# Optimization experiments

Measured on AMD Instinct MI355X. Metric: run time of the kernel, lower is better.

Reference implementation:

```python
import jax, jax.numpy as jnp
import numpy as np

L, B, D, N = 2048, 8, 1024, 64

def setup_inputs() -> dict:
    key = jax.random.key(0)
    ks = jax.random.split(key, 6)
    return {
        "x": jax.random.normal(ks[0], (L, B, D), dtype=jnp.float32),
        "damping_factor": jax.random.normal(ks[1], (D, N, 1), dtype=jnp.float32),
        "decay_factor": jax.random.normal(ks[2], (D, N, 1), dtype=jnp.float32),
        "ema_expansion_matrix": jax.random.normal(ks[3], (D, N, 1), dtype=jnp.float32),
        "kernel_projection_matrix": jax.random.normal(ks[4], (D, N), dtype=jnp.float32),
        "residual_weight": jax.random.normal(ks[5], (D,), dtype=jnp.float32),
    }

def reference(x, damping_factor, decay_factor, ema_expansion_matrix,
              kernel_projection_matrix, residual_weight):
    seq_len, bsz, dim = x.shape
    ndim = damping_factor.shape[1]
    # --- kernel synthesis (training path, unidirectional) ---
    damping = jax.nn.sigmoid(damping_factor)           # (D, N, 1)
    decay = jax.nn.sigmoid(decay_factor)               # (D, N, 1)
    prev_w = 1.0 - damping * decay                     # (D, N, 1), in (0,1)
    t = jnp.arange(seq_len, dtype=jnp.float32)[None, None, :]  # (1,1,L)
    vander = t * jnp.log(prev_w)                       # (D, N, L)
    kernel_vals = damping * ema_expansion_matrix * jnp.exp(vander)  # (D,N,L)
    kernel = jnp.einsum('dnl,dn->dl', kernel_vals, kernel_projection_matrix)
    kernel = kernel * np.float32(1.0 / np.sqrt(ndim))  # (D, L)
    # --- residual + FFT long convolution ---
    residual = x * residual_weight                     # (L, B, D)
    x_conv = jnp.transpose(x, (1, 2, 0))               # (B, D, L)
    n_fft = 2 * seq_len
    x_fft = jnp.fft.rfft(x_conv, n=n_fft)              # (B, D, n/2+1)
    k_fft = jnp.fft.rfft(kernel, n=n_fft)              # (D, n/2+1)
    conv = jnp.fft.irfft(x_fft * k_fft, n=n_fft)[..., :seq_len]  # (B, D, L)
    ema_out = jnp.transpose(conv, (2, 0, 1))           # (L, B, D)
    return jax.nn.silu(ema_out + residual)
```

## Files before the change

kernel.cpp:

```cpp
#include <hip/hip_runtime.h>
#include <hip/hip_bf16.h>


#define BSZ 8
#define DIM 1024
#define ND 64
#define BD 8192
#define SEGS 4
#define SEGLEN 512
#define CH1 64
#define CPS1 8
#define TD 16
#define XP1 68
#define NCH2 16
#define YP2 17

typedef short bf16x8 __attribute__((ext_vector_type(8)));
typedef float f32x4 __attribute__((ext_vector_type(4)));
union BF8 { uint32_t u[4]; bf16x8 v; };
#define MFMA __builtin_amdgcn_mfma_f32_16x16x32_bf16

__device__ __forceinline__ uint32_t pk_bf16(float a, float b) {
    __hip_bfloat162 h2 = __float22bfloat162_rn(make_float2(a, b));
    uint32_t u; __builtin_memcpy(&u, &h2, 4);
    return u;
}

__device__ __forceinline__ void block_sync_lds() {
    asm volatile("s_waitcnt lgkmcnt(0)" ::: "memory");
    __builtin_amdgcn_s_barrier();
    asm volatile("" ::: "memory");
}

__global__ __launch_bounds__(128, 8) void mega_pass1(
    const float* __restrict__ x,
    const float* __restrict__ dfp,
    const float* __restrict__ cfp,
    ushort* __restrict__ S)
{
    __shared__ float xb[2][TD * XP1];

    const int tid = threadIdx.x;
    const int lane = tid & 63;
    const int wv = tid >> 6;
    const int q   = (lane & 3) | (((lane >> 3) & 1) << 2);
    const int col = wv * 8 + ((lane >> 2) & 1) + ((lane >> 4) & 3) * 2;
    const int blk = blockIdx.x;
    const int dt  = blk & 63;
    const int b   = (blk >> 6) & 7;
    const int seg = blk >> 9;
    const int d   = dt * TD + col;

    float w[8];
    {
        const int pb = d * ND + q * 8;
        const float4 df0 = *(const float4*)(dfp + pb);
        const float4 df1 = *(const float4*)(dfp + pb + 4);
        const float4 cf0 = *(const float4*)(cfp + pb);
        const float4 cf1 = *(const float4*)(cfp + pb + 4);
        const float dfv[8] = {df0.x, df0.y, df0.z, df0.w, df1.x, df1.y, df1.z, df1.w};
        const float cfv[8] = {cf0.x, cf0.y, cf0.z, cf0.w, cf1.x, cf1.y, cf1.z, cf1.w};
        #pragma unroll
        for (int i = 0; i < 8; ++i) {
            const float sd = 1.0f / (1.0f + __expf(-dfv[i]));
            const float sc = 1.0f / (1.0f + __expf(-cfv[i]));
            w[i] = 1.0f - sd * sc;
        }
    }

    const int r0 = tid >> 2;
    const int c4 = (tid & 3) * 4;
    const float* xg = x + (size_t)(seg * SEGLEN) * BD + b * DIM + dt * TD;

    float4 nx0 = *(const float4*)(xg + (size_t)r0 * BD + c4);
    float4 nx1 = *(const float4*)(xg + (size_t)(r0 + 32) * BD + c4);

    float h[8];
    #pragma unroll
    for (int i = 0; i < 8; ++i) h[i] = 0.0f;

    for (int g = 0; g < CPS1; ++g) {
        float* xbuf = xb[g & 1];
        const float nv0[4] = {nx0.x, nx0.y, nx0.z, nx0.w};
        const float nv1[4] = {nx1.x, nx1.y, nx1.z, nx1.w};
        #pragma unroll
        for (int e = 0; e < 4; ++e) {
            xbuf[(c4 + e) * XP1 + r0]      = nv0[e];
            xbuf[(c4 + e) * XP1 + r0 + 32] = nv1[e];
        }
        if (g + 1 < CPS1) {
            nx0 = *(const float4*)(xg + (size_t)((g + 1) * CH1 + r0) * BD + c4);
            nx1 = *(const float4*)(xg + (size_t)((g + 1) * CH1 + r0 + 32) * BD + c4);
        }
        block_sync_lds();

        const float* xcol = xbuf + col * XP1;
        #pragma unroll 2
        for (int t8 = 0; t8 < 8; ++t8) {
            const float4 tva = *(const float4*)(xcol + t8 * 8);
            const float4 tvb = *(const float4*)(xcol + t8 * 8 + 4);
            const float tvs[8] = {tva.x, tva.y, tva.z, tva.w,
                                  tvb.x, tvb.y, tvb.z, tvb.w};
            #pragma unroll
            for (int k = 0; k < 8; ++k) {
                const float xv = tvs[k];
                #pragma unroll
                for (int i = 0; i < 8; ++i) h[i] = fmaf(w[i], h[i], xv);
            }
        }
    }

    const size_t sb = ((size_t)(seg * BSZ + b) * 64 + dt) * 1024 + col * 64 + q * 8;
    uint32_t pk[4] = {pk_bf16(h[0], h[1]), pk_bf16(h[2], h[3]),
                      pk_bf16(h[4], h[5]), pk_bf16(h[6], h[7])};
    *(uint4*)(S + sb) = make_uint4(pk[0], pk[1], pk[2], pk[3]);
}

__global__ __launch_bounds__(1024, 4) void mega_pass2(
    const float* __restrict__ x,
    const float* __restrict__ dfp,
    const float* __restrict__ cfp,
    const float* __restrict__ emp,
    const float* __restrict__ pjp,
    const float* __restrict__ rwp,
    const ushort* __restrict__ S,
    float* __restrict__ out)
{
    __shared__ __align__(16) ushort   xbh[2][TD * 8 * 32];
    __shared__ __align__(16) float    yt[2][256 * YP2];
    __shared__ __align__(16) uint32_t hbq[16 * 256];
    __shared__ __align__(8)  float2   pclw[16 * 64];
    __shared__ float kap[16 * 32];

    const int tid = threadIdx.x;
    const int tl  = tid & 63;
    const int wv  = tid >> 6;
    const int c   = tl & 15;
    const int g   = tl >> 4;
    const int cq  = c & 7;
    const int hf  = c >> 3;
    const int blk = blockIdx.x;
    const int seg = blk >> 6;
    const int dt  = blk & 63;
    const int d0  = dt * TD;
    const int d   = d0 + wv;

    {
        const int pidx = d * ND + tl;
        const float sd = 1.0f / (1.0f + __expf(-dfp[pidx]));
        const float sc = 1.0f / (1.0f + __expf(-cfp[pidx]));
        const float wn = 1.0f - sd * sc;
        const float cn = sd * emp[pidx] * pjp[pidx] * 0.125f;
        pclw[wv * 64 + tl] = make_float2(cn, log2f(wn));
    }
    const float rwd = rwp[d];

    const int drow = tid & 15;
    const int bq   = ((tid >> 4) & 1) | (((tid >> 6) & 1) << 1) | (((tid >> 8) & 1) << 2);
    const int l4g  = ((tid >> 5) & 1) | (((tid >> 7) & 1) << 1) | (((tid >> 9) & 1) << 2);
    const int Gst  = l4g >> 1;
    const int Hst  = l4g & 1;
    const int Kst  = ((bq >> 1) & 3) ^ (drow & 3);
    const int xwoff = (drow * 8 + bq) * 32 + ((Gst ^ Kst) << 3) + Hst * 4;
    const float* xgs = x + (size_t)(seg * SEGLEN + 4 * l4g) * BD + bq * DIM + d0 + drow;
    float nx0 = xgs[0];
    float nx1 = xgs[(size_t)BD];
    float nx2 = xgs[(size_t)2 * BD];
    float nx3 = xgs[(size_t)3 * BD];

    const int dq  = tid & 3;
    const int b_s = (tid >> 2) & 7;
    const int u_s = (tid >> 5) & 7;
    const int r_s = tid >> 8;
    const int yrow = b_s + 8 * u_s + 64 * r_s;
    const int lam  = 4 * u_s + r_s;

    float lw16[16];
    #pragma unroll
    for (int T = 0; T < 4; ++T)
        #pragma unroll
        for (int r = 0; r < 4; ++r)
            lw16[T * 4 + r] = pclw[wv * 64 + 16 * T + 4 * g + r].y;

    float h[16];
    #pragma unroll
    for (int i = 0; i < 16; ++i) h[i] = 0.0f;
    if (seg > 0) {
        float w512[16];
        #pragma unroll
        for (int i = 0; i < 16; ++i) w512[i] = exp2f(512.0f * lw16[i]);
        for (int sp = 0; sp < seg; ++sp) {
            const size_t sbase = ((size_t)(sp * BSZ + cq) * 64 + dt) * 1024 + wv * 64;
            #pragma unroll
            for (int T = 0; T < 4; ++T) {
                const uint2 u = *(const uint2*)(S + sbase + 16 * T + 4 * g);
                const float s0 = __uint_as_float(u.x << 16);
                const float s1 = __uint_as_float(u.x & 0xFFFF0000u);
                const float s2 = __uint_as_float(u.y << 16);
                const float s3 = __uint_as_float(u.y & 0xFFFF0000u);
                h[T*4+0] = fmaf(w512[T*4+0], h[T*4+0], s0);
                h[T*4+1] = fmaf(w512[T*4+1], h[T*4+1], s1);
                h[T*4+2] = fmaf(w512[T*4+2], h[T*4+2], s2);
                h[T*4+3] = fmaf(w512[T*4+3], h[T*4+3], s3);
            }
        }
    }
    float w32[16];
    #pragma unroll
    for (int i = 0; i < 16; ++i) w32[i] = exp2f(32.0f * lw16[i]);

    BF8 Vf[4], T2f[2][2], Kf[2];
    #pragma unroll
    for (int T = 0; T < 4; ++T) {
        const float2 pcl = pclw[wv * 64 + 16 * T + c];
        const float winv = exp2f(-pcl.y);
        float ve = exp2f((float)(31 - 8 * g) * pcl.y);
        float vv[8];
        #pragma unroll
        for (int e = 0; e < 8; ++e) { vv[e] = ve; ve *= winv; }
        #pragma unroll
        for (int j = 0; j < 4; ++j) Vf[T].u[j] = pk_bf16(vv[2*j], vv[2*j+1]);
    }
    #pragma unroll
    for (int Tk = 0; Tk < 2; ++Tk) {
        float2 m8[8];
        #pragma unroll
        for (int e = 0; e < 8; ++e) m8[e] = pclw[wv * 64 + 32 * Tk + 8 * g + e];
        #pragma unroll
        for (int Tj = 0; Tj < 2; ++Tj) {
            const float jf = (float)(16 * Tj + c + 1);
            float tv[8];
            #pragma unroll
            for (int e = 0; e < 8; ++e) tv[e] = m8[e].x * exp2f(jf * m8[e].y);
            #pragma unroll
            for (int j = 0; j < 4; ++j) T2f[Tj][Tk].u[j] = pk_bf16(tv[2*j], tv[2*j+1]);
        }
    }
    {
        const int p = tl >> 1, half = tl & 1;
        float acc = 0.0f;
        for (int i = 0; i < 32; ++i) {
            const float2 pc = pclw[wv * 64 + half * 32 + i];
            acc = fmaf(pc.x, exp2f((float)p * pc.y), acc);
        }
        const int prt = __builtin_amdgcn_update_dpp(0, __float_as_int(acc), 0xB1, 0xF, 0xF, true);
        acc += __int_as_float(prt);
        if (!half) kap[wv * 32 + p] = acc;
    }
    #pragma unroll
    for (int Tj = 0; Tj < 2; ++Tj) {
        float kv[8];
        #pragma unroll
        for (int e = 0; e < 8; ++e) {
            const int pp = 16 * Tj + c - 8 * g - e;
            float kv_;
            if (pp > 0)       kv_ = kap[wv * 32 + pp];
            else if (pp == 0) kv_ = kap[wv * 32] + rwd;
            else              kv_ = 0.0f;
            kv[e] = kv_;
        }
        #pragma unroll
        for (int j = 0; j < 4; ++j) Kf[Tj].u[j] = pk_bf16(kv[2*j], kv[2*j+1]);
    }

    const int Krd   = ((cq >> 1) & 3) ^ (wv & 3);
    const int xroff = (wv * 8 + cq) * 32 + ((g ^ Krd) << 3);
    const int swzc = ((c & 3) << 3) | (((c >> 2) & 1) << 2);
    uint32_t* hbw = hbq + wv * 256 + cq * 32;
    float* ogbase = out + (size_t)(seg * SEGLEN) * BD + d0;
    const f32x4 zf = {0.0f, 0.0f, 0.0f, 0.0f};

    if (hf == 0) {
        #pragma unroll
        for (int T = 0; T < 4; ++T) {
            const int p0 = 8 * T + 2 * g;
            *(uint2*)(&hbw[p0 ^ swzc]) =
                make_uint2(pk_bf16(h[4*T+0], h[4*T+1]), pk_bf16(h[4*T+2], h[4*T+3]));
        }
    }
    BF8 hB0, hB1;
    {
        const uint4 a  = *(const uint4*)(&hbw[(4 * g) ^ swzc]);
        const uint4 b2 = *(const uint4*)(&hbw[(16 + 4 * g) ^ swzc]);
        hB0.u[0]=a.x;  hB0.u[1]=a.y;  hB0.u[2]=a.z;  hB0.u[3]=a.w;
        hB1.u[0]=b2.x; hB1.u[1]=b2.y; hB1.u[2]=b2.z; hB1.u[3]=b2.w;
    }
    {
        *(uint2*)(&xbh[0][xwoff]) = make_uint2(pk_bf16(nx0, nx1), pk_bf16(nx2, nx3));
        const float* xp = xgs + (size_t)32 * BD;
        nx0 = xp[0]; nx1 = xp[(size_t)BD]; nx2 = xp[(size_t)2*BD]; nx3 = xp[(size_t)3*BD];
    }
    block_sync_lds();

    for (int ch = 0; ch < NCH2; ++ch) {
        BF8 xB;
        xB.v = *(const bf16x8*)(&xbh[ch & 1][xroff]);

        if (ch + 1 < NCH2) {
            *(uint2*)(&xbh[(ch + 1) & 1][xwoff]) =
                make_uint2(pk_bf16(nx0, nx1), pk_bf16(nx2, nx3));
            if (ch + 2 < NCH2) {
                const float* xp = xgs + (size_t)(ch + 2) * 32 * BD;
                nx0 = xp[0]; nx1 = xp[(size_t)BD]; nx2 = xp[(size_t)2*BD]; nx3 = xp[(size_t)3*BD];
            }
        }
        if (ch > 0) {
            const float* yprev = yt[(ch - 1) & 1];
            float ov[4];
            #pragma unroll
            for (int e = 0; e < 4; ++e) ov[e] = yprev[yrow * YP2 + 4 * dq + e];
            *(float4*)(ogbase + (size_t)((ch - 1) * 32 + lam) * BD + b_s * DIM + 4 * dq) =
                make_float4(ov[0], ov[1], ov[2], ov[3]);
        }

        f32x4 y0 = MFMA(Kf[0].v, xB.v, zf, 0, 0, 0);
        f32x4 y1 = MFMA(Kf[1].v, xB.v, zf, 0, 0, 0);
        y0 = MFMA(T2f[0][0].v, hB0.v, y0, 0, 0, 0);
        y1 = MFMA(T2f[1][0].v, hB0.v, y1, 0, 0, 0);
        y0 = MFMA(T2f[0][1].v, hB1.v, y0, 0, 0, 0);
        y1 = MFMA(T2f[1][1].v, hB1.v, y1, 0, 0, 0);
        #pragma unroll
        for (int T = 0; T < 4; ++T) {
            const f32x4 U = MFMA(Vf[T].v, xB.v, zf, 0, 0, 0);
            h[4*T+0] = fmaf(w32[4*T+0], h[4*T+0], U[0]);
            h[4*T+1] = fmaf(w32[4*T+1], h[4*T+1], U[1]);
            h[4*T+2] = fmaf(w32[4*T+2], h[4*T+2], U[2]);
            h[4*T+3] = fmaf(w32[4*T+3], h[4*T+3], U[3]);
        }
        if (hf == 0) {
            #pragma unroll
            for (int T = 0; T < 4; ++T) {
                const int p0 = 8 * T + 2 * g;
                *(uint2*)(&hbw[p0 ^ swzc]) =
                    make_uint2(pk_bf16(h[4*T+0], h[4*T+1]), pk_bf16(h[4*T+2], h[4*T+3]));
            }
        }
        {
            const uint4 a  = *(const uint4*)(&hbw[(4 * g) ^ swzc]);
            const uint4 b2 = *(const uint4*)(&hbw[(16 + 4 * g) ^ swzc]);
            hB0.u[0]=a.x;  hB0.u[1]=a.y;  hB0.u[2]=a.z;  hB0.u[3]=a.w;
            hB1.u[0]=b2.x; hB1.u[1]=b2.y; hB1.u[2]=b2.z; hB1.u[3]=b2.w;
        }

        {
            float* ycur = yt[ch & 1];
            const f32x4 yy = hf ? y1 : y0;
            #pragma unroll
            for (int r = 0; r < 4; ++r) {
                const float v = yy[r];
                const float sv = v / (1.0f + __expf(-v));
                ycur[(cq + 8 * g + 32 * hf + 64 * r) * YP2 + wv] = sv;
            }
        }
        block_sync_lds();
    }

    {
        const float* yprev = yt[(NCH2 - 1) & 1];
        float ov[4];
        #pragma unroll
        for (int e = 0; e < 4; ++e) ov[e] = yprev[yrow * YP2 + 4 * dq + e];
        *(float4*)(ogbase + (size_t)((NCH2 - 1) * 32 + lam) * BD + b_s * DIM + 4 * dq) =
            make_float4(ov[0], ov[1], ov[2], ov[3]);
    }
}

extern "C" void kernel_launch(void* const* d_in, const int* in_sizes, int n_in,
                              void* d_out, int out_size, void* d_ws, size_t ws_size,
                              hipStream_t stream) {
    const float* x  = (const float*)d_in[0];
    const float* df = (const float*)d_in[1];
    const float* cf = (const float*)d_in[2];
    const float* em = (const float*)d_in[3];
    const float* pj = (const float*)d_in[4];
    const float* rw = (const float*)d_in[5];
    float* out = (float*)d_out;
    ushort* S  = (ushort*)d_ws;

    mega_pass1<<<dim3((SEGS - 1) * BSZ * 64), dim3(128), 0, stream>>>(x, df, cf, S);
    mega_pass2<<<dim3(SEGS * 64), dim3(1024), 0, stream>>>(x, df, cf, em, pj, rw, S, out);
}
```

Measured before the change: 75.99 us.

## Preload whole x segment into LDS and store outputs directly without barriers

Stages all 16 chunks of the x segment into LDS as bf16 in one upfront loop, replacing the double-buffered register prefetch. The staging tile for the output transpose is removed: each lane writes its SiLU results straight to global memory. This takes out the per-chunk block barriers and LDS round-trips. In exchange, LDS use grows to roughly 150KB per block. Global stores become 4-byte scattered writes with a DIM stride instead of coalesced float4 stores, and x loads no longer overlap with the MFMA loop.

```diff
diff --git a/kernel.cpp b/kernel.cpp
--- a/kernel.cpp
+++ b/kernel.cpp
@@ -13,7 +13,6 @@
 #define TD 16
 #define XP1 68
 #define NCH2 16
-#define YP2 17
 
 typedef short bf16x8 __attribute__((ext_vector_type(8)));
 typedef float f32x4 __attribute__((ext_vector_type(4)));
@@ -126,8 +125,7 @@
     const ushort* __restrict__ S,
     float* __restrict__ out)
 {
-    __shared__ __align__(16) ushort   xbh[2][TD * 8 * 32];
-    __shared__ __align__(16) float    yt[2][256 * YP2];
+    __shared__ __align__(16) ushort   xbh[NCH2 * TD * 8 * 32];
     __shared__ __align__(16) uint32_t hbq[16 * 256];
     __shared__ __align__(8)  float2   pclw[16 * 64];
     __shared__ float kap[16 * 32];
@@ -163,17 +161,16 @@
     const int Kst  = ((bq >> 1) & 3) ^ (drow & 3);
     const int xwoff = (drow * 8 + bq) * 32 + ((Gst ^ Kst) << 3) + Hst * 4;
     const float* xgs = x + (size_t)(seg * SEGLEN + 4 * l4g) * BD + bq * DIM + d0 + drow;
-    float nx0 = xgs[0];
-    float nx1 = xgs[(size_t)BD];
-    float nx2 = xgs[(size_t)2 * BD];
-    float nx3 = xgs[(size_t)3 * BD];
-
-    const int dq  = tid & 3;
-    const int b_s = (tid >> 2) & 7;
-    const int u_s = (tid >> 5) & 7;
-    const int r_s = tid >> 8;
-    const int yrow = b_s + 8 * u_s + 64 * r_s;
-    const int lam  = 4 * u_s + r_s;
+
+    #pragma unroll 4
+    for (int ch = 0; ch < NCH2; ++ch) {
+        const float* xp = xgs + (size_t)ch * 32 * BD;
+        const float a0 = xp[0];
+        const float a1 = xp[(size_t)BD];
+        const float a2 = xp[(size_t)2 * BD];
+        const float a3 = xp[(size_t)3 * BD];
+        *(uint2*)(&xbh[ch * 4096 + xwoff]) = make_uint2(pk_bf16(a0, a1), pk_bf16(a2, a3));
+    }
 
     float lw16[16];
     #pragma unroll
@@ -263,13 +260,9 @@
         for (int j = 0; j < 4; ++j) Kf[Tj].u[j] = pk_bf16(kv[2*j], kv[2*j+1]);
     }
 
-    const int Krd   = ((cq >> 1) & 3) ^ (wv & 3);
-    const int xroff = (wv * 8 + cq) * 32 + ((g ^ Krd) << 3);
     const int swzc = ((c & 3) << 3) | (((c >> 2) & 1) << 2);
     uint32_t* hbw = hbq + wv * 256 + cq * 32;
-    float* ogbase = out + (size_t)(seg * SEGLEN) * BD + d0;
     const f32x4 zf = {0.0f, 0.0f, 0.0f, 0.0f};
-
     if (hf == 0) {
         #pragma unroll
         for (int T = 0; T < 4; ++T) {
@@ -285,33 +278,16 @@
         hB0.u[0]=a.x;  hB0.u[1]=a.y;  hB0.u[2]=a.z;  hB0.u[3]=a.w;
         hB1.u[0]=b2.x; hB1.u[1]=b2.y; hB1.u[2]=b2.z; hB1.u[3]=b2.w;
     }
-    {
-        *(uint2*)(&xbh[0][xwoff]) = make_uint2(pk_bf16(nx0, nx1), pk_bf16(nx2, nx3));
-        const float* xp = xgs + (size_t)32 * BD;
-        nx0 = xp[0]; nx1 = xp[(size_t)BD]; nx2 = xp[(size_t)2*BD]; nx3 = xp[(size_t)3*BD];
-    }
+
     block_sync_lds();
+
+    const int Krd   = ((cq >> 1) & 3) ^ (wv & 3);
+    const int xroff = (wv * 8 + cq) * 32 + ((g ^ Krd) << 3);
+    float* ogl = out + (size_t)(seg * SEGLEN + 16 * hf + 4 * g) * BD + cq * DIM + d;
 
     for (int ch = 0; ch < NCH2; ++ch) {
         BF8 xB;
-        xB.v = *(const bf16x8*)(&xbh[ch & 1][xroff]);
-
-        if (ch + 1 < NCH2) {
-            *(uint2*)(&xbh[(ch + 1) & 1][xwoff]) =
-                make_uint2(pk_bf16(nx0, nx1), pk_bf16(nx2, nx3));
-            if (ch + 2 < NCH2) {
-                const float* xp = xgs + (size_t)(ch + 2) * 32 * BD;
-                nx0 = xp[0]; nx1 = xp[(size_t)BD]; nx2 = xp[(size_t)2*BD]; nx3 = xp[(size_t)3*BD];
-            }
-        }
-        if (ch > 0) {
-            const float* yprev = yt[(ch - 1) & 1];
-            float ov[4];
-            #pragma unroll
-            for (int e = 0; e < 4; ++e) ov[e] = yprev[yrow * YP2 + 4 * dq + e];
-            *(float4*)(ogbase + (size_t)((ch - 1) * 32 + lam) * BD + b_s * DIM + 4 * dq) =
-                make_float4(ov[0], ov[1], ov[2], ov[3]);
-        }
+        xB.v = *(const bf16x8*)(&xbh[ch * 4096 + xroff]);
 
         f32x4 y0 = MFMA(Kf[0].v, xB.v, zf, 0, 0, 0);
         f32x4 y1 = MFMA(Kf[1].v, xB.v, zf, 0, 0, 0);
@@ -343,25 +319,15 @@
         }
 
         {
-            float* ycur = yt[ch & 1];
             const f32x4 yy = hf ? y1 : y0;
+            float* op = ogl + (size_t)ch * 32 * BD;
             #pragma unroll
             for (int r = 0; r < 4; ++r) {
                 const float v = yy[r];
                 const float sv = v / (1.0f + __expf(-v));
-                ycur[(cq + 8 * g + 32 * hf + 64 * r) * YP2 + wv] = sv;
+                op[(size_t)r * BD] = sv;
             }
         }
-        block_sync_lds();
-    }
-
-    {
-        const float* yprev = yt[(NCH2 - 1) & 1];
-        float ov[4];
-        #pragma unroll
-        for (int e = 0; e < 4; ++e) ov[e] = yprev[yrow * YP2 + 4 * dq + e];
-        *(float4*)(ogbase + (size_t)((NCH2 - 1) * 32 + lam) * BD + b_s * DIM + 4 * dq) =
-            make_float4(ov[0], ov[1], ov[2], ov[3]);
     }
 }
 
```

Result: slower. 144.2 us (+89.8%).
